# Kernel tuning notes

Measured on AMD Instinct MI355X. Metric: run time of the kernel, lower is better.

Reference implementation:

```python
import jax, jax.numpy as jnp
import numpy as np

# norse default LIFParameters (dt=1e-3): tau_mem_inv=100, tau_syn_inv=200, v_leak=0, v_reset=0
DT = 1e-3
TAU_MEM_INV = 100.0
TAU_SYN_INV = 200.0
V_TH_ENC = 1.0   # encoder built with default LIFParameters -> v_th=1.0
V_TH = 0.33      # LIF cells built with v_th=0.33
SEQ_LEN = 24
ALPHA = 100.0    # SuperSpike surrogate-gradient slope (norse 'super' method)

@jax.custom_vjp
def heaviside(x):
    # forward: hard threshold; backward: SuperSpike surrogate 1/(alpha*|x|+1)^2
    return (x > 0).astype(x.dtype)

def _hv_fwd(x):
    return heaviside(x), x

def _hv_bwd(x, g):
    return (g / (ALPHA * jnp.abs(x) + 1.0) ** 2,)

heaviside.defvjp(_hv_fwd, _hv_bwd)


def setup_inputs() -> dict:
    key = jax.random.key(0)
    ks = jax.random.split(key, 6)
    B, F, H, C = 4096, 1024, 256, 10
    def lin(k, fan_out, fan_in):  # torch Linear default init (no bias)
        bound = 1.0 / np.sqrt(fan_in)
        return jax.random.uniform(k, (fan_out, fan_in), jnp.float32, -bound, bound)
    return {
        "x": jax.random.normal(ks[0], (B, F), jnp.float32),
        "W1": lin(ks[1], H, F),
        "W2": lin(ks[2], H, H),
        "W3": lin(ks[3], H, H),
        "Wout": jax.random.normal(ks[4], (C, H), jnp.float32) * np.sqrt(2.0 / H),
        "feature_scalar": jnp.ones((1,), jnp.float32),
        "encoder_scalar": jnp.ones((1,), jnp.float32),
    }


def _lif_step(z_in, v, i):
    # norse lif_feed_forward_step: decay v/i from old state, spike, reset, then inject input into i
    v_dec = v + DT * TAU_MEM_INV * (-v + i)
    i_dec = i * (1.0 - DT * TAU_SYN_INV)
    z = heaviside(v_dec - V_TH)
    v_new = (1.0 - z) * v_dec  # v_reset = 0
    i_new = i_dec + z_in
    return z, v_new, i_new


def reference(x, W1, W2, W3, Wout, feature_scalar, encoder_scalar):
    B, F = x.shape
    H = W1.shape[0]
    C = Wout.shape[0]
    current = 2.0 * feature_scalar * x  # constant injected current, [B, F]
    z0 = lambda d: jnp.zeros((B, d), x.dtype)
    init = (z0(F), z0(H), z0(H), z0(H), z0(H), z0(H), z0(H), z0(C), z0(C))

    def step(state, _):
        v_enc, v1, i1, v2, i2, v3, i3, v_li, i_li = state
        # ConstantCurrentLIFEncoder (lif_current_encoder, v_th=1.0)
        v_enc = v_enc + DT * TAU_MEM_INV * (-v_enc + current)
        s = heaviside(v_enc - V_TH_ENC)
        v_enc = v_enc - s * v_enc  # reset to 0
        z = 5.0 * encoder_scalar * s
        # three Linear(no bias)+LIF stages (dropout in eval mode = identity)
        z, v1, i1 = _lif_step(1.2 * (z @ W1.T), v1, i1)
        z, v2, i2 = _lif_step(1.2 * (z @ W2.T), v2, i2)
        z, v3, i3 = _lif_step(1.2 * (z @ W3.T), v3, i3)
        # LILinearCell: leaky integrator readout
        v_li = v_li + DT * TAU_MEM_INV * (-v_li + i_li)
        i_li = i_li * (1.0 - DT * TAU_SYN_INV) + z @ Wout.T
        return (v_enc, v1, i1, v2, i2, v3, i3, v_li, i_li), None

    final, _ = jax.lax.scan(step, init, None, length=SEQ_LEN)
    return final[7]  # decode = voltages[-1], shape [B, n_classes]
```

## Files before the change

kernel.cpp:

```cpp
#include <hip/hip_runtime.h>

using u16 = unsigned short;
using u32 = unsigned int;
using u64 = unsigned long long;

typedef _Float16 half8 __attribute__((ext_vector_type(8)));
typedef float  f32x4 __attribute__((ext_vector_type(4)));
typedef u32    u32x4 __attribute__((ext_vector_type(4)));
typedef u32    u32x2 __attribute__((ext_vector_type(2)));

#define T_STEPS 24
#define NB 4096
#define NF 1024
#define NH 256
#define NCLS 10

static __device__ __forceinline__ void f16split(float w, u16& hi, u16& lo) {
  _Float16 h = (_Float16)w;
  float hf = (float)h;
  if (__builtin_fabsf(hf) < 6.103515625e-05f) { h = (_Float16)0.0f; hf = 0.0f; }
  float r = __fmul_rn(__fsub_rn(w, hf), 4096.0f);
  _Float16 l = (_Float16)r;
  hi = __builtin_bit_cast(u16, h);
  lo = __builtin_bit_cast(u16, l);
}

__global__ __launch_bounds__(256) void k_prep(const float* __restrict__ W1,
                                              const float* __restrict__ W2,
                                              const float* __restrict__ W3,
                                              u16* __restrict__ W1hl,
                                              u16* __restrict__ W2hl,
                                              u16* __restrict__ W3hl) {
  int blk = blockIdx.x, tid = threadIdx.x;
  const float* src; u16* dst; int K; int g;
  if (blk < 1024)      { src = W1; dst = W1hl; K = 1024; g = blk * 256 + tid; }
  else if (blk < 1280) { src = W2; dst = W2hl; K = 256;  g = (blk - 1024) * 256 + tid; }
  else                 { src = W3; dst = W3hl; K = 256;  g = (blk - 1280) * 256 + tid; }
  int n = g / K, k = g - n * K;
  u16 hi, lo;
  f16split(src[g], hi, lo);
  int p = k >> 6, j = k & 63;
  u16* d = dst + (size_t)n * 2 * K + p * 128 + j;
  d[0] = hi;
  d[64] = lo;
}

template <int NSC, int ASTRIDE>
__device__ __forceinline__ void mega_phase(u16* __restrict__ Bs,
                                           const u32* __restrict__ alds,
                                           const u16* __restrict__ wsrc,
                                           u32* __restrict__ zdst,
                                           float scale,
                                           int wid, int lane, int wm, int wn) {
  constexpr int KTOT = NSC * 64;

  const int bsh   = (lane >> 4) * 8;
  const int rbase = (wn * 64 + (lane & 15)) * 64;
  int pu8[2];
  #pragma unroll
  for (int h = 0; h < 2; ++h)
    pu8[h] = (((4 * h + (lane >> 4)) ^ (lane & 7)) * 8);
  const int sunit = ((lane & 7) ^ (lane >> 3)) * 8;
  const u16* gs = wsrc + (size_t)(wid * 32 + (lane >> 3)) * KTOT + sunit;
  const int ldsw = wid * 2048;

  auto stage = [&](int s, int b) {
    const u16* g = gs + s * 64;
    #pragma unroll
    for (int r = 0; r < 4; ++r)
      __builtin_amdgcn_global_load_lds(
          (const __attribute__((address_space(1))) u32*)(g + (size_t)r * 8 * KTOT),
          (__attribute__((address_space(3))) u32*)&Bs[b * 16384 + ldsw + r * 512],
          16, 0, 0);
  };

  int arow[3];
  #pragma unroll
  for (int ms = 0; ms < 3; ++ms)
    arow[ms] = (wm * 48 + ms * 16 + (lane & 15)) * ASTRIDE;

  auto expand = [&](u32 word) -> half8 {
    u32 by = (word >> bsh) & 0xFFu;
    u32 sp = by * 0x8001u;
    u32x4 d;
    d.x = (sp & 0x10001u) * 0x3C00u;
    d.y = ((sp >> 2) & 0x10001u) * 0x3C00u;
    d.z = ((sp >> 4) & 0x10001u) * 0x3C00u;
    d.w = ((sp >> 6) & 0x10001u) * 0x3C00u;
    return __builtin_bit_cast(half8, d);
  };

  const _Float16 scl = (_Float16)2.44140625e-4f;
  const half8 sc8 = {scl, scl, scl, scl, scl, scl, scl, scl};

  f32x4 acc[3][4];
  #pragma unroll
  for (int ms = 0; ms < 3; ++ms)
    #pragma unroll
    for (int ns = 0; ns < 4; ++ns)
      #pragma unroll
      for (int i = 0; i < 4; ++i) acc[ms][ns][i] = 0.0f;

  stage(0, 0);

  half8 afr[3][2];
  #pragma unroll 2
  for (int s = 0; s < NSC; ++s) {
    __syncthreads();
    if ((s & 1) == 0) {
      u32x2 bw[3];
      #pragma unroll
      for (int ms = 0; ms < 3; ++ms)
        bw[ms] = *(const u32x2*)(alds + arow[ms] + s);
      if (s + 1 < NSC) stage(s + 1, (s + 1) & 1);
      #pragma unroll
      for (int ms = 0; ms < 3; ++ms) {
        afr[ms][0] = expand(bw[ms].x);
        afr[ms][1] = expand(bw[ms].y);
      }
    } else {
      if (s + 1 < NSC) stage(s + 1, (s + 1) & 1);
      #pragma unroll
      for (int ms = 0; ms < 3; ++ms) {
        afr[ms][0] = afr[ms][0] * sc8;
        afr[ms][1] = afr[ms][1] * sc8;
      }
    }

    const int bufo = (s & 1) * 16384;
    #pragma unroll
    for (int h = 0; h < 2; ++h) {
      #pragma unroll
      for (int ns = 0; ns < 4; ++ns) {
        half8 bfr = *(const half8*)&Bs[bufo + rbase + ns * 1024 + pu8[h]];
        #pragma unroll
        for (int ms = 0; ms < 3; ++ms)
          acc[ms][ns] = __builtin_amdgcn_mfma_f32_16x16x32_f16(afr[ms][h], bfr,
                                                               acc[ms][ns], 0, 0, 0);
      }
    }
  }
  __syncthreads();

  float* reg = (float*)Bs + wid * 1600;
  const int q   = lane >> 4, c16 = lane & 15;
  const int b2  = lane >> 5, c   = lane & 31;

  #pragma unroll
  for (int r = 0; r < 2; ++r) {
    #pragma unroll
    for (int ms = 0; ms < 3; ++ms)
      #pragma unroll
      for (int j = 0; j < 2; ++j)
        #pragma unroll
        for (int i = 0; i < 4; ++i)
          reg[(ms * 16 + q * 4 + i) * 33 + j * 16 + c16] =
              __fmul_rn(scale, acc[ms][2 * r + j][i]);
    float v = 0.0f, ii = 0.0f;
    u32 zw = 0;
    #pragma unroll
    for (int t = 0; t < T_STEPS; ++t) {
      float cv = reg[(b2 * 24 + t) * 33 + c];
      float vdec = __fadd_rn(v, __fmul_rn(0.1f, __fsub_rn(ii, v)));
      float idec = __fmul_rn(0.8f, ii);
      bool z = vdec > 0.33f;
      v = z ? 0.0f : vdec;
      ii = __fadd_rn(idec, cv);
      zw |= ((u32)z) << t;
    }
    #pragma unroll
    for (int t = 0; t < T_STEPS; ++t) {
      u64 m = __ballot((zw >> t) & 1u);
      if (c == 0)
        zdst[((wm * 2 + b2) * 24 + t) * 8 + wn * 2 + r] = (u32)(m >> (b2 * 32));
    }
  }
  __syncthreads();
}

__global__ __launch_bounds__(512, 4) void k_mega(const float* __restrict__ x,
                                                 const float* __restrict__ fsp,
                                                 const float* __restrict__ esp,
                                                 const u16* __restrict__ W1hl,
                                                 const u16* __restrict__ W2hl,
                                                 const u16* __restrict__ W3hl,
                                                 const float* __restrict__ Wo,
                                                 float* __restrict__ out) {
  __shared__ __align__(16) u16 Bs[2 * 16384];
  __shared__ u32 zE[96 * 34];
  __shared__ u32 zA[96 * 8];

  const int tid  = threadIdx.x;
  const int wid  = tid >> 6;
  const int lane = tid & 63;
  const int wm   = wid & 1;
  const int wn   = wid >> 1;
  const int b0   = blockIdx.x * 4;

  {
    const int bb = wid >> 1;
    const int fbase = (wid & 1) * 512;
    const float c2 = __fmul_rn(2.0f, fsp[0]);
    float cur[8], v[8];
    #pragma unroll
    for (int j = 0; j < 8; ++j) {
      cur[j] = __fmul_rn(c2, x[(size_t)(b0 + bb) * 1024 + fbase + j * 64 + lane]);
      v[j] = 0.0f;
    }
    #pragma unroll
    for (int t = 0; t < T_STEPS; ++t) {
      #pragma unroll
      for (int j = 0; j < 8; ++j) {
        v[j] = __fadd_rn(v[j], __fmul_rn(0.1f, __fsub_rn(cur[j], v[j])));
        bool s = v[j] > 1.0f;
        if (s) v[j] = 0.0f;
        u64 m = __ballot(s);
        if (lane == 0) {
          int w0 = (bb * 24 + t) * 34 + (fbase >> 5) + 2 * j;
          zE[w0] = (u32)m;
          zE[w0 + 1] = (u32)(m >> 32);
        }
      }
    }
  }
  __syncthreads();

  const float s1 = __fmul_rn(1.2f, __fmul_rn(5.0f, esp[0]));
  mega_phase<32, 34>(Bs, zE, W1hl, zA, s1, wid, lane, wm, wn);
  mega_phase<8, 8>(Bs, zA, W2hl, zE, 1.2f, wid, lane, wm, wn);
  mega_phase<8, 8>(Bs, zE, W3hl, zA, 1.2f, wid, lane, wm, wn);

  {
    float* s_lds = (float*)Bs;
    #pragma unroll
    for (int r = 0; r < 2; ++r) {
      const int idx = tid + r * 512;
      const int b = idx >> 8, h = idx & 255;
      const u32* zp = zA + (b * 24) * 8 + (h >> 5);
      const int bit = h & 31;
      float p9 = 1.0f, p8 = 1.0f, s = 0.0f;
      #pragma unroll
      for (int e = 0; e < 24; ++e) {
        const float a = __fsub_rn(p9, p8);
        const u32 word = zp[(23 - e) * 8];
        s = __fadd_rn(s, ((word >> bit) & 1u) ? a : 0.0f);
        p9 = __fmul_rn(p9, 0.9f);
        p8 = __fmul_rn(p8, 0.8f);
      }
      s_lds[idx] = s;
    }
    __syncthreads();
    #pragma unroll
    for (int oi = 0; oi < 5; ++oi) {
      const int o = wid * 5 + oi;
      const int b = o / 10, cls = o - (o / 10) * 10;
      f32x4 sv = *(const f32x4*)&s_lds[b * 256 + lane * 4];
      f32x4 wv = *(const f32x4*)&Wo[(size_t)cls * 256 + lane * 4];
      float d = __fadd_rn(__fadd_rn(__fmul_rn(sv.x, wv.x), __fmul_rn(sv.y, wv.y)),
                          __fadd_rn(__fmul_rn(sv.z, wv.z), __fmul_rn(sv.w, wv.w)));
      #pragma unroll
      for (int off2 = 32; off2 >= 1; off2 >>= 1)
        d = __fadd_rn(d, __shfl_down(d, off2));
      if (lane == 0) out[(size_t)(b0 + b) * NCLS + cls] = d;
    }
  }
}

extern "C" void kernel_launch(void* const* d_in, const int* in_sizes, int n_in,
                              void* d_out, int out_size, void* d_ws, size_t ws_size,
                              hipStream_t stream) {
  const float* x  = (const float*)d_in[0];
  const float* W1 = (const float*)d_in[1];
  const float* W2 = (const float*)d_in[2];
  const float* W3 = (const float*)d_in[3];
  const float* Wo = (const float*)d_in[4];
  const float* fs = (const float*)d_in[5];
  const float* es = (const float*)d_in[6];

  char* ws = (char*)d_ws;
  const size_t off_w1 = 0;
  const size_t off_w2 = off_w1 + (size_t)NH * 2 * NF * 2;
  const size_t off_w3 = off_w2 + (size_t)NH * 2 * NH * 2;
  const size_t need   = off_w3 + (size_t)NH * 2 * NH * 2;
  if (ws_size < need) return;

  u16* W1hl = (u16*)(ws + off_w1);
  u16* W2hl = (u16*)(ws + off_w2);
  u16* W3hl = (u16*)(ws + off_w3);

  k_prep<<<dim3(1536), dim3(256), 0, stream>>>(W1, W2, W3, W1hl, W2hl, W3hl);
  k_mega<<<dim3(NB / 4), dim3(512), 0, stream>>>(x, fs, es, W1hl, W2hl, W3hl, Wo,
                                                 (float*)d_out);
}
```

Measured before the change: 233.0 us.

## Load weight fragments directly from global into registers, drop LDS staging

```diff
diff --git a/kernel.cpp b/kernel.cpp
--- a/kernel.cpp
+++ b/kernel.cpp
@@ -46,7 +46,7 @@
 }
 
 template <int NSC, int ASTRIDE>
-__device__ __forceinline__ void mega_phase(u16* __restrict__ Bs,
+__device__ __forceinline__ void mega_phase(float* __restrict__ regbuf,
                                            const u32* __restrict__ alds,
                                            const u16* __restrict__ wsrc,
                                            u32* __restrict__ zdst,
@@ -54,25 +54,10 @@
                                            int wid, int lane, int wm, int wn) {
   constexpr int KTOT = NSC * 64;
 
-  const int bsh   = (lane >> 4) * 8;
-  const int rbase = (wn * 64 + (lane & 15)) * 64;
-  int pu8[2];
-  #pragma unroll
-  for (int h = 0; h < 2; ++h)
-    pu8[h] = (((4 * h + (lane >> 4)) ^ (lane & 7)) * 8);
-  const int sunit = ((lane & 7) ^ (lane >> 3)) * 8;
-  const u16* gs = wsrc + (size_t)(wid * 32 + (lane >> 3)) * KTOT + sunit;
-  const int ldsw = wid * 2048;
-
-  auto stage = [&](int s, int b) {
-    const u16* g = gs + s * 64;
-    #pragma unroll
-    for (int r = 0; r < 4; ++r)
-      __builtin_amdgcn_global_load_lds(
-          (const __attribute__((address_space(1))) u32*)(g + (size_t)r * 8 * KTOT),
-          (__attribute__((address_space(3))) u32*)&Bs[b * 16384 + ldsw + r * 512],
-          16, 0, 0);
-  };
+  const int q   = lane >> 4;
+  const int bsh = q * 8;
+
+  const u16* bb = wsrc + (size_t)(wn * 64 + (lane & 15)) * KTOT + q * 8;
 
   int arow[3];
   #pragma unroll
@@ -101,50 +86,64 @@
       #pragma unroll
       for (int i = 0; i < 4; ++i) acc[ms][ns][i] = 0.0f;
 
-  stage(0, 0);
+  half8 bfA[2][4], bfB[2][4];
+  auto loadA = [&](int s) {
+    #pragma unroll
+    for (int h = 0; h < 2; ++h)
+      #pragma unroll
+      for (int ns = 0; ns < 4; ++ns)
+        bfA[h][ns] = *(const half8*)(bb + (size_t)ns * 16 * KTOT + s * 64 + h * 32);
+  };
+  auto loadB = [&](int s) {
+    #pragma unroll
+    for (int h = 0; h < 2; ++h)
+      #pragma unroll
+      for (int ns = 0; ns < 4; ++ns)
+        bfB[h][ns] = *(const half8*)(bb + (size_t)ns * 16 * KTOT + s * 64 + h * 32);
+  };
+
+  loadA(0);
 
   half8 afr[3][2];
-  #pragma unroll 2
-  for (int s = 0; s < NSC; ++s) {
-    __syncthreads();
-    if ((s & 1) == 0) {
-      u32x2 bw[3];
-      #pragma unroll
-      for (int ms = 0; ms < 3; ++ms)
-        bw[ms] = *(const u32x2*)(alds + arow[ms] + s);
-      if (s + 1 < NSC) stage(s + 1, (s + 1) & 1);
-      #pragma unroll
-      for (int ms = 0; ms < 3; ++ms) {
-        afr[ms][0] = expand(bw[ms].x);
-        afr[ms][1] = expand(bw[ms].y);
-      }
-    } else {
-      if (s + 1 < NSC) stage(s + 1, (s + 1) & 1);
-      #pragma unroll
-      for (int ms = 0; ms < 3; ++ms) {
-        afr[ms][0] = afr[ms][0] * sc8;
-        afr[ms][1] = afr[ms][1] * sc8;
-      }
-    }
-
-    const int bufo = (s & 1) * 16384;
-    #pragma unroll
-    for (int h = 0; h < 2; ++h) {
-      #pragma unroll
-      for (int ns = 0; ns < 4; ++ns) {
-        half8 bfr = *(const half8*)&Bs[bufo + rbase + ns * 1024 + pu8[h]];
+  for (int m = 0; m < NSC / 2; ++m) {
+    const int s = 2 * m;
+    u32x2 bw[3];
+    #pragma unroll
+    for (int ms = 0; ms < 3; ++ms)
+      bw[ms] = *(const u32x2*)(alds + arow[ms] + s);
+    loadB(s + 1);
+    #pragma unroll
+    for (int ms = 0; ms < 3; ++ms) {
+      afr[ms][0] = expand(bw[ms].x);
+      afr[ms][1] = expand(bw[ms].y);
+    }
+    #pragma unroll
+    for (int h = 0; h < 2; ++h)
+      #pragma unroll
+      for (int ns = 0; ns < 4; ++ns)
         #pragma unroll
         for (int ms = 0; ms < 3; ++ms)
-          acc[ms][ns] = __builtin_amdgcn_mfma_f32_16x16x32_f16(afr[ms][h], bfr,
+          acc[ms][ns] = __builtin_amdgcn_mfma_f32_16x16x32_f16(afr[ms][h], bfA[h][ns],
                                                                acc[ms][ns], 0, 0, 0);
-      }
-    }
-  }
-  __syncthreads();
-
-  float* reg = (float*)Bs + wid * 1600;
-  const int q   = lane >> 4, c16 = lane & 15;
-  const int b2  = lane >> 5, c   = lane & 31;
+    if (s + 2 < NSC) loadA(s + 2);
+    #pragma unroll
+    for (int ms = 0; ms < 3; ++ms) {
+      afr[ms][0] = afr[ms][0] * sc8;
+      afr[ms][1] = afr[ms][1] * sc8;
+    }
+    #pragma unroll
+    for (int h = 0; h < 2; ++h)
+      #pragma unroll
+      for (int ns = 0; ns < 4; ++ns)
+        #pragma unroll
+        for (int ms = 0; ms < 3; ++ms)
+          acc[ms][ns] = __builtin_amdgcn_mfma_f32_16x16x32_f16(afr[ms][h], bfB[h][ns],
+                                                               acc[ms][ns], 0, 0, 0);
+  }
+
+  float* reg = regbuf + wid * 1600;
+  const int c16 = lane & 15;
+  const int b2  = lane >> 5, c = lane & 31;
 
   #pragma unroll
   for (int r = 0; r < 2; ++r) {
@@ -186,7 +185,7 @@
                                                  const u16* __restrict__ W3hl,
                                                  const float* __restrict__ Wo,
                                                  float* __restrict__ out) {
-  __shared__ __align__(16) u16 Bs[2 * 16384];
+  __shared__ __align__(16) float regbuf[8 * 1600];
   __shared__ u32 zE[96 * 34];
   __shared__ u32 zA[96 * 8];
 
@@ -226,12 +225,12 @@
   __syncthreads();
 
   const float s1 = __fmul_rn(1.2f, __fmul_rn(5.0f, esp[0]));
-  mega_phase<32, 34>(Bs, zE, W1hl, zA, s1, wid, lane, wm, wn);
-  mega_phase<8, 8>(Bs, zA, W2hl, zE, 1.2f, wid, lane, wm, wn);
-  mega_phase<8, 8>(Bs, zE, W3hl, zA, 1.2f, wid, lane, wm, wn);
+  mega_phase<32, 34>(regbuf, zE, W1hl, zA, s1, wid, lane, wm, wn);
+  mega_phase<8, 8>(regbuf, zA, W2hl, zE, 1.2f, wid, lane, wm, wn);
+  mega_phase<8, 8>(regbuf, zE, W3hl, zA, 1.2f, wid, lane, wm, wn);
 
   {
-    float* s_lds = (float*)Bs;
+    float* s_lds = regbuf;
     #pragma unroll
     for (int r = 0; r < 2; ++r) {
       const int idx = tid + r * 512;
```

Result: slower. 470.7 us (+102.0%).
